# Performance work log

Measured on AMD Instinct MI355X. Metric: run time of the kernel, lower is better.

## Reference

```python
import jax, jax.numpy as jnp
from jax import lax
import numpy as np

B, T, D = 8, 2048, 1024
EPS = 1e-8


def zc_rms(x, g):
    x0 = x - jnp.mean(x, axis=-1, keepdims=True)
    return x0 * jax.lax.rsqrt(jnp.mean(x0 * x0, axis=-1, keepdims=True) + EPS) * g


def l2norm(x):
    return x * jax.lax.rsqrt(jnp.sum(x * x, axis=-1, keepdims=True) + EPS)


def dwconv3(x, w, b):
    # x: [B, T, D]; w: [D, 3] depthwise kernel; b: [D]
    xc = jnp.transpose(x, (0, 2, 1))  # [B, D, T]
    y = lax.conv_general_dilated(xc, w[:, None, :], window_strides=(1,),
                                 padding=[(1, 1)],
                                 dimension_numbers=('NCH', 'OIH', 'NCH'),
                                 feature_group_count=w.shape[0])
    return jnp.transpose(y + b[:, None], (0, 2, 1))  # [B, T, D]


def setup_inputs() -> dict:
    key = jax.random.key(0)
    ks = jax.random.split(key, 16)
    s = 1.0 / np.sqrt(D)
    inp = {
        'x': jax.random.normal(ks[0], (B, T, D), jnp.float32),
        'g1': jnp.ones((D,), jnp.float32),
        'Wq': jax.random.normal(ks[1], (D, D), jnp.float32) * s,
        'bq': jnp.zeros((D,), jnp.float32),
        'Wk': jax.random.normal(ks[2], (D, D), jnp.float32) * s,
        'bk': jnp.zeros((D,), jnp.float32),
        'Wv': jax.random.normal(ks[3], (D, D), jnp.float32) * s,
        'bv': jnp.zeros((D,), jnp.float32),
        'wqc': jax.random.normal(ks[4], (D, 3), jnp.float32) * 0.5,
        'bqc': jnp.zeros((D,), jnp.float32),
        'wkc': jax.random.normal(ks[5], (D, 3), jnp.float32) * 0.5,
        'bkc': jnp.zeros((D,), jnp.float32),
        'wvc': jax.random.normal(ks[6], (D, 3), jnp.float32) * 0.5,
        'bvc': jnp.zeros((D,), jnp.float32),
        'Wa': jax.random.normal(ks[7], (D, D), jnp.float32) * s,
        'ba': jnp.zeros((D,), jnp.float32),
        'Wb': jax.random.normal(ks[8], (D, D), jnp.float32) * s,
        'bb': jnp.zeros((D,), jnp.float32),
        'g2': jnp.ones((D,), jnp.float32),
        'Wp': jax.random.normal(ks[9], (D, D), jnp.float32) * s,
        'bp': jnp.zeros((D,), jnp.float32),
    }
    return inp


def reference(x, g1, Wq, bq, Wk, bk, Wv, bv, wqc, bqc, wkc, bkc, wvc, bvc,
              Wa, ba, Wb, bb, g2, Wp, bp):
    h = zc_rms(x, g1)
    q = jax.nn.sigmoid(dwconv3(h @ Wq + bq, wqc, bqc))
    k = jax.nn.sigmoid(dwconv3(h @ Wk + bk, wkc, bkc))
    v = jax.nn.sigmoid(dwconv3(h @ Wv + bv, wvc, bvc))
    q, k = l2norm(q), l2norm(k)
    delta = q * (k * v)
    delta = jnp.tanh(x @ Wa + ba) * delta + (x @ Wb + bb)
    dhat = zc_rms(delta, g2) @ Wp + bp
    # dropout is identity in eval mode
    return x + jax.nn.sigmoid(jax.nn.silu(dhat)) * dhat
```

## Files before the change

### kernel.cpp

```cpp
#include <hip/hip_runtime.h>
#include <stdint.h>

#define DD 1024
#define TT 2048
#define BBATCH 8
#define MM (BBATCH*TT)

typedef unsigned short u16;
typedef unsigned int   u32;

typedef __attribute__((ext_vector_type(8))) __bf16 bf16x8;
typedef __attribute__((ext_vector_type(4))) float  floatx4;
typedef __attribute__((ext_vector_type(4))) unsigned short u16x4;
typedef __attribute__((ext_vector_type(8))) unsigned short u16x8;
typedef __attribute__((ext_vector_type(4))) unsigned int   u32x4;

__device__ __forceinline__ float b2f(u16 v){
    u32 x = ((u32)v) << 16;
    return __builtin_bit_cast(float, x);
}
__device__ __forceinline__ u16 f2b(float f){
    u32 u = __builtin_bit_cast(u32, f);
    u32 r = (u + 0x7fffu + ((u >> 16) & 1u)) >> 16;
    return (u16)r;
}
__device__ __forceinline__ float sigf(float x){
    return 1.0f / (1.0f + __expf(-x));
}
__device__ __forceinline__ float tanhfast(float x){
    float e = __expf(2.0f * x);
    return 1.0f - 2.0f / (e + 1.0f);
}

__device__ __forceinline__ void g2l16(const u16* g, u16* l){
    __builtin_amdgcn_global_load_lds(
        (const __attribute__((address_space(1))) u32*)g,
        (__attribute__((address_space(3))) u32*)l, 16, 0, 0);
}

__device__ __forceinline__ u32 lds_u32(const u16* p){
    return (u32)(size_t)(const __attribute__((address_space(3))) u16*)p;
}

template<int OFF>
__device__ __forceinline__ bf16x8 dsr(u32 addr){
    u32x4 d;
    asm volatile("ds_read_b128 %0, %1 offset:%2" : "=v"(d) : "v"(addr), "i"(OFF));
    return __builtin_bit_cast(bf16x8, d);
}

template<int BASE>
__device__ __forceinline__ void rd_a8(bf16x8 (&arr)[8], u32 a){
    arr[0]=dsr<BASE+0>(a);    arr[1]=dsr<BASE+64>(a);
    arr[2]=dsr<BASE+2048>(a); arr[3]=dsr<BASE+2112>(a);
    arr[4]=dsr<BASE+4096>(a); arr[5]=dsr<BASE+4160>(a);
    arr[6]=dsr<BASE+6144>(a); arr[7]=dsr<BASE+6208>(a);
}
template<int BASE>
__device__ __forceinline__ void rd_b4(bf16x8 (&arr)[4], u32 a){
    arr[0]=dsr<BASE+0>(a);    arr[1]=dsr<BASE+64>(a);
    arr[2]=dsr<BASE+2048>(a); arr[3]=dsr<BASE+2112>(a);
}

__device__ __forceinline__ void load4bf(const u16* p, float* o){
    u16x4 v = *(const u16x4*)p;
    o[0] = b2f(v.x); o[1] = b2f(v.y); o[2] = b2f(v.z); o[3] = b2f(v.w);
}

__device__ __forceinline__ void wave_reduce2(float& a, float& b){
    #pragma unroll
    for (int m = 32; m; m >>= 1){
        a += __shfl_xor(a, m, 64);
        b += __shfl_xor(b, m, 64);
    }
}

__device__ __forceinline__ void block_reduce2(float& a, float& b, float* red, int tid){
    #pragma unroll
    for (int off = 32; off; off >>= 1){
        a += __shfl_down(a, off, 64);
        b += __shfl_down(b, off, 64);
    }
    __syncthreads();
    if ((tid & 63) == 0){ red[tid >> 6] = a; red[4 + (tid >> 6)] = b; }
    __syncthreads();
    a = red[0] + red[1] + red[2] + red[3];
    b = red[4] + red[5] + red[6] + red[7];
}

__global__ __launch_bounds__(256) void transpose_w(
    const float* __restrict__ s0, const float* __restrict__ s1, const float* __restrict__ s2,
    const float* __restrict__ s3, const float* __restrict__ s4, const float* __restrict__ s5,
    u16* __restrict__ dst_base)
{
    __shared__ u16 tile[32][33];
    const float* srcs[6] = {s0, s1, s2, s3, s4, s5};
    const int z = blockIdx.z;
    const float* src = srcs[z];
    u16* dst = dst_base + (size_t)z * (DD * (size_t)DD);
    const int tx = threadIdx.x, ty = threadIdx.y;
    const int x = blockIdx.x * 32 + tx;
    #pragma unroll
    for (int i = 0; i < 4; i++){
        int y = blockIdx.y * 32 + ty + i * 8;
        tile[ty + i * 8][tx] = f2b(src[(size_t)y * DD + x]);
    }
    __syncthreads();
    const int x2 = blockIdx.y * 32 + tx;
    #pragma unroll
    for (int i = 0; i < 4; i++){
        int y2 = blockIdx.x * 32 + ty + i * 8;
        dst[(size_t)y2 * DD + x2] = tile[tx][ty + i * 8];
    }
}

__global__ __launch_bounds__(256) void prep_wc(
    const float* __restrict__ w0, const float* __restrict__ w1, const float* __restrict__ w2,
    float* __restrict__ wcT)
{
    const float* srcs[3] = {w0, w1, w2};
    const int s = blockIdx.x / 3, tap = blockIdx.x % 3;
    #pragma unroll
    for (int i = 0; i < 4; i++){
        int d = threadIdx.x + i * 256;
        wcT[(s * 3 + tap) * DD + d] = srcs[s][d * 3 + tap];
    }
}

__global__ __launch_bounds__(256) void prep_rows(
    const float* __restrict__ in, const float* __restrict__ g,
    u16* __restrict__ xb, u16* __restrict__ h)
{
    const int tid = threadIdx.x;
    const int w = tid >> 6, lane = tid & 63;
    const int row = blockIdx.x * 4 + w;
    const int d0 = lane * 16;
    const size_t base = (size_t)row * DD + d0;

    float v[16];
    #pragma unroll
    for (int c = 0; c < 4; c++){
        floatx4 t = *(const floatx4*)(in + base + c * 4);
        v[c*4+0] = t.x; v[c*4+1] = t.y; v[c*4+2] = t.z; v[c*4+3] = t.w;
    }
    u16x8 x0, x1;
    #pragma unroll
    for (int j = 0; j < 8; j++){ x0[j] = f2b(v[j]); x1[j] = f2b(v[8+j]); }
    *(u16x8*)(xb + base)     = x0;
    *(u16x8*)(xb + base + 8) = x1;

    float s1 = 0.f, s2 = 0.f;
    #pragma unroll
    for (int j = 0; j < 16; j++){ s1 += v[j]; s2 += v[j]*v[j]; }
    wave_reduce2(s1, s2);
    const float mu = s1 * (1.0f / DD);
    const float ms = fmaxf(s2 * (1.0f / DD) - mu * mu, 0.0f);
    const float sc = rsqrtf(ms + 1e-8f);

    u16x8 o0, o1;
    #pragma unroll
    for (int j = 0; j < 8; j++)  o0[j] = f2b((v[j]     - mu) * sc * g[d0 + j]);
    #pragma unroll
    for (int j = 0; j < 8; j++)  o1[j] = f2b((v[8 + j] - mu) * sc * g[d0 + 8 + j]);
    *(u16x8*)(h + base)     = o0;
    *(u16x8*)(h + base + 8) = o1;
}

struct GemmPtrs {
    const u16*   A[5];
    const u16*   W[5];
    const float* bias[5];
    u16*         out[5];
};

#define BAR()   asm volatile("s_barrier" ::: "memory")
#define LGKM0() asm volatile("s_waitcnt lgkmcnt(0)" ::: "memory")
#define VM8()   asm volatile("s_waitcnt vmcnt(8)" ::: "memory")
#define SB0()   __builtin_amdgcn_sched_barrier(0)
#define PRIO1() __builtin_amdgcn_s_setprio(1)
#define PRIO0() __builtin_amdgcn_s_setprio(0)

template<int IH, int JH>
__device__ __forceinline__ void mm8(floatx4 (&acc)[8][4], const bf16x8 (&af)[8], const bf16x8 (&bf)[4]){
    #pragma unroll
    for (int kk = 0; kk < 2; kk++)
        #pragma unroll
        for (int i = 0; i < 4; i++)
            #pragma unroll
            for (int j = 0; j < 2; j++)
                acc[IH*4+i][JH*2+j] = __builtin_amdgcn_mfma_f32_16x16x32_bf16(
                    af[i*2+kk], bf[j*2+kk], acc[IH*4+i][JH*2+j], 0, 0, 0);
}

template<int MODE>
__global__ __launch_bounds__(512, 2) void gemm_bf16(
    GemmPtrs ptrs, const float* __restrict__ xres, float* __restrict__ dout)
{
    __shared__ alignas(16) u16 lds[65536];

    const int z = blockIdx.z;
    const u16*   __restrict__ A    = ptrs.A[z];
    const u16*   __restrict__ W    = ptrs.W[z];
    const float* __restrict__ bias = ptrs.bias[z];
    u16* __restrict__ Cout = ptrs.out[z];

    const int tid  = threadIdx.x;
    const int wave = tid >> 6, lane = tid & 63;
    const int quad = lane >> 4, l16 = lane & 15;
    const int wrow = wave >> 2, wcol = wave & 3;
    const int bm = blockIdx.x * 256;
    const int bn = blockIdx.y * 256;

    const int coloff = ((tid & 7) * 8) ^ (((tid >> 5) & 1) << 4);
    const u16* srcA = A + (size_t)(bm + (tid >> 3)) * DD + coloff;
    const u16* srcB = W + (size_t)(bn + (tid >> 3)) * DD + coloff;

    #define STAGE_A(T,H) do{ \
        u16* _d = &lds[(((T)&1)*2 + (H))*8192 + tid*8]; \
        const u16* _g = srcA + (size_t)(H)*128*DD + (size_t)(((T)&15)*64); \
        g2l16(_g, _d); g2l16(_g + (size_t)64*DD, _d + 4096); }while(0)
    #define STAGE_B(T,H) do{ \
        u16* _d = &lds[32768 + (((T)&1)*2 + (H))*8192 + tid*8]; \
        const u16* _g = srcB + (size_t)(H)*128*DD + (size_t)(((T)&15)*64); \
        g2l16(_g, _d); g2l16(_g + (size_t)64*DD, _d + 4096); }while(0)

    const u32 swz = (u32)((quad * 16) ^ (((l16 >> 2) & 1) << 5));
    const u32 lbase = lds_u32(&lds[0]);
    u32 addr_a = lbase + (u32)(wrow * 8192 + l16 * 128) + swz;
    u32 addr_b = lbase + 65536u + (u32)(wcol * 4096 + l16 * 128) + swz;

    floatx4 acc[8][4];
    #pragma unroll
    for (int i = 0; i < 8; i++)
        #pragma unroll
        for (int j = 0; j < 4; j++)
            acc[i][j] = (floatx4){0.f, 0.f, 0.f, 0.f};

    STAGE_A(0,0); STAGE_B(0,0); STAGE_B(0,1); STAGE_A(0,1); STAGE_A(1,0); STAGE_B(1,0);
    VM8(); BAR();

    bf16x8 af0[8], af1[8], bf0[4], bf1[4];

    for (int t = 0; t < 16; ++t){
        rd_a8<0>(af0, addr_a);
        rd_b4<0>(bf0, addr_b);
        STAGE_B(t+1, 1);
        BAR(); LGKM0(); SB0();
        PRIO1(); mm8<0,0>(acc, af0, bf0); PRIO0(); SB0();
        VM8(); BAR();
        rd_b4<16384>(bf1, addr_b);
        STAGE_A(t+1, 1);
        BAR(); LGKM0(); SB0();
        PRIO1(); mm8<0,1>(acc, af0, bf1); PRIO0(); SB0();
        VM8(); BAR();
        rd_a8<16384>(af1, addr_a);
        STAGE_A(t+2, 0);
        BAR(); LGKM0(); SB0();
        PRIO1(); mm8<1,0>(acc, af1, bf0); PRIO0(); SB0();
        STAGE_B(t+2, 0);
        PRIO1(); mm8<1,1>(acc, af1, bf1); PRIO0(); SB0();
        VM8(); BAR();
        addr_a ^= 32768u; addr_b ^= 32768u;
    }

    #undef STAGE_A
    #undef STAGE_B

    float bj[4];
    #pragma unroll
    for (int j = 0; j < 4; j++)
        bj[j] = bias[bn + (j >= 2 ? 128 : 0) + wcol * 32 + (j & 1) * 16 + l16];

    #pragma unroll
    for (int i = 0; i < 8; i++){
        const int row0 = bm + (i >= 4 ? 128 : 0) + wrow * 64 + (i & 3) * 16 + quad * 4;
        #pragma unroll
        for (int j = 0; j < 4; j++){
            const int col = bn + (j >= 2 ? 128 : 0) + wcol * 32 + (j & 1) * 16 + l16;
            #pragma unroll
            for (int r = 0; r < 4; r++){
                size_t idx = (size_t)(row0 + r) * DD + col;
                float zv = acc[i][j][r] + bj[j];
                if (MODE == 0){
                    Cout[idx] = f2b(zv);
                } else {
                    float sl = zv * sigf(zv);
                    dout[idx] = xres[idx] + sigf(sl) * zv;
                }
            }
        }
    }
}

__global__ __launch_bounds__(256) void mid_fuse(
    const u16* __restrict__ q0, const u16* __restrict__ k0, const u16* __restrict__ v0,
    const u16* __restrict__ a0, const u16* __restrict__ b0,
    const float* __restrict__ wcT,
    const float* __restrict__ bqc, const float* __restrict__ bkc, const float* __restrict__ bvc,
    const float* __restrict__ g2, u16* __restrict__ uout)
{
    __shared__ float red[8];
    const int row = blockIdx.x;
    const int t   = row & (TT - 1);
    const int tid = threadIdx.x;
    const int d0  = tid * 4;
    const size_t base = (size_t)row * DD + d0;
    const bool hm = (t > 0), hp = (t < TT - 1);

    float q[4], k[4], v[4];
    {
        const u16*   srcs[3] = {q0, k0, v0};
        const float* bs[3]   = {bqc, bkc, bvc};
        float* outs[3]       = {q, k, v};
        #pragma unroll
        for (int s = 0; s < 3; s++){
            float cm[4], cc[4], cp[4];
            load4bf(srcs[s] + base, cc);
            if (hm) load4bf(srcs[s] + base - DD, cm);
            else { cm[0]=0.f; cm[1]=0.f; cm[2]=0.f; cm[3]=0.f; }
            if (hp) load4bf(srcs[s] + base + DD, cp);
            else { cp[0]=0.f; cp[1]=0.f; cp[2]=0.f; cp[3]=0.f; }
            const float* wt = wcT + s * 3 * DD + d0;
            const float* bb = bs[s] + d0;
            #pragma unroll
            for (int j = 0; j < 4; j++){
                float y = cm[j] * wt[j] + cc[j] * wt[DD + j] + cp[j] * wt[2 * DD + j] + bb[j];
                outs[s][j] = sigf(y);
            }
        }
    }

    float sq = 0.f, sk = 0.f;
    #pragma unroll
    for (int j = 0; j < 4; j++){ sq += q[j] * q[j]; sk += k[j] * k[j]; }
    block_reduce2(sq, sk, red, tid);
    const float rq = rsqrtf(sq + 1e-8f), rk = rsqrtf(sk + 1e-8f);

    float av[4], bv[4];
    load4bf(a0 + base, av);
    load4bf(b0 + base, bv);

    float dl[4], s1 = 0.f, s2 = 0.f;
    #pragma unroll
    for (int j = 0; j < 4; j++){
        float d = (q[j] * rq) * (k[j] * rk) * v[j];
        d = tanhfast(av[j]) * d + bv[j];
        dl[j] = d; s1 += d; s2 += d * d;
    }
    block_reduce2(s1, s2, red, tid);
    const float mu = s1 * (1.0f / DD);
    const float ms = fmaxf(s2 * (1.0f / DD) - mu * mu, 0.0f);
    const float sc = rsqrtf(ms + 1e-8f);

    u16x4 ov;
    ov.x = f2b((dl[0] - mu) * sc * g2[d0 + 0]);
    ov.y = f2b((dl[1] - mu) * sc * g2[d0 + 1]);
    ov.z = f2b((dl[2] - mu) * sc * g2[d0 + 2]);
    ov.w = f2b((dl[3] - mu) * sc * g2[d0 + 3]);
    *(u16x4*)(uout + base) = ov;
}

extern "C" void kernel_launch(void* const* d_in, const int* in_sizes, int n_in,
                              void* d_out, int out_size, void* d_ws, size_t ws_size,
                              hipStream_t stream)
{
    const float* x   = (const float*)d_in[0];
    const float* g1  = (const float*)d_in[1];
    const float* Wq  = (const float*)d_in[2];
    const float* bq  = (const float*)d_in[3];
    const float* Wk  = (const float*)d_in[4];
    const float* bk  = (const float*)d_in[5];
    const float* Wv  = (const float*)d_in[6];
    const float* bv  = (const float*)d_in[7];
    const float* wqc = (const float*)d_in[8];
    const float* bqc = (const float*)d_in[9];
    const float* wkc = (const float*)d_in[10];
    const float* bkc = (const float*)d_in[11];
    const float* wvc = (const float*)d_in[12];
    const float* bvc = (const float*)d_in[13];
    const float* Wa  = (const float*)d_in[14];
    const float* ba  = (const float*)d_in[15];
    const float* Wb  = (const float*)d_in[16];
    const float* bb  = (const float*)d_in[17];
    const float* g2  = (const float*)d_in[18];
    const float* Wp  = (const float*)d_in[19];
    const float* bp  = (const float*)d_in[20];

    u16* ws = (u16*)d_ws;
    const size_t WSZ = (size_t)DD * DD;
    const size_t TSZ = (size_t)MM * DD;
    u16* WT = ws;
    float* wcT = (float*)(ws + 6 * WSZ);
    u16* xb = ws + 6 * WSZ + 32768;
    u16* h  = xb + TSZ;
    u16* q0 = h  + TSZ;
    u16* k0 = q0 + TSZ;
    u16* v0 = k0 + TSZ;
    u16* a0 = v0 + TSZ;
    u16* b0 = a0 + TSZ;
    u16* u  = h;

    transpose_w<<<dim3(32, 32, 6), dim3(32, 8, 1), 0, stream>>>(Wq, Wk, Wv, Wa, Wb, Wp, WT);
    prep_wc<<<dim3(9), dim3(256), 0, stream>>>(wqc, wkc, wvc, wcT);
    prep_rows<<<dim3(MM / 4), dim3(256), 0, stream>>>(x, g1, xb, h);

    GemmPtrs p0;
    p0.A[0] = h;  p0.W[0] = WT + 0 * WSZ; p0.bias[0] = bq; p0.out[0] = q0;
    p0.A[1] = h;  p0.W[1] = WT + 1 * WSZ; p0.bias[1] = bk; p0.out[1] = k0;
    p0.A[2] = h;  p0.W[2] = WT + 2 * WSZ; p0.bias[2] = bv; p0.out[2] = v0;
    p0.A[3] = xb; p0.W[3] = WT + 3 * WSZ; p0.bias[3] = ba; p0.out[3] = a0;
    p0.A[4] = xb; p0.W[4] = WT + 4 * WSZ; p0.bias[4] = bb; p0.out[4] = b0;
    gemm_bf16<0><<<dim3(64, 4, 5), dim3(512), 0, stream>>>(p0, nullptr, nullptr);

    mid_fuse<<<dim3(MM), dim3(256), 0, stream>>>(q0, k0, v0, a0, b0,
                                                 wcT, bqc, bkc, bvc, g2, u);

    GemmPtrs p1;
    for (int i = 0; i < 5; i++){ p1.A[i] = u; p1.W[i] = WT + 5 * WSZ; p1.bias[i] = bp; p1.out[i] = nullptr; }
    gemm_bf16<1><<<dim3(64, 4, 1), dim3(512), 0, stream>>>(p1, x, (float*)d_out);
}
```

Measured before the change: 470.3 us.

## Use full XOR LDS swizzle, prefetch next fragments, and trim GEMM barriers

The GEMM's LDS layout changes to a full 8-way XOR swizzle on 16-byte chunks, with two base addresses per wave, to reduce bank conflicts on ds_read_b128. Fragment reads for the next k-step are issued during the current MFMA phases, so LDS latency overlaps compute. Several barriers are removed and the global-load wait tightens from vmcnt(8) to vmcnt(4). This risks race conditions on the double-buffered LDS if the barrier removal breaks ordering, and adds register pressure from the live prefetched fragments.

```diff
diff --git a/kernel.cpp b/kernel.cpp
--- a/kernel.cpp
+++ b/kernel.cpp
@@ -50,16 +50,16 @@
 }
 
 template<int BASE>
-__device__ __forceinline__ void rd_a8(bf16x8 (&arr)[8], u32 a){
-    arr[0]=dsr<BASE+0>(a);    arr[1]=dsr<BASE+64>(a);
-    arr[2]=dsr<BASE+2048>(a); arr[3]=dsr<BASE+2112>(a);
-    arr[4]=dsr<BASE+4096>(a); arr[5]=dsr<BASE+4160>(a);
-    arr[6]=dsr<BASE+6144>(a); arr[7]=dsr<BASE+6208>(a);
+__device__ __forceinline__ void rd_a8(bf16x8 (&arr)[8], u32 a0, u32 a1){
+    arr[0]=dsr<BASE+0>(a0);    arr[1]=dsr<BASE+0>(a1);
+    arr[2]=dsr<BASE+2048>(a0); arr[3]=dsr<BASE+2048>(a1);
+    arr[4]=dsr<BASE+4096>(a0); arr[5]=dsr<BASE+4096>(a1);
+    arr[6]=dsr<BASE+6144>(a0); arr[7]=dsr<BASE+6144>(a1);
 }
 template<int BASE>
-__device__ __forceinline__ void rd_b4(bf16x8 (&arr)[4], u32 a){
-    arr[0]=dsr<BASE+0>(a);    arr[1]=dsr<BASE+64>(a);
-    arr[2]=dsr<BASE+2048>(a); arr[3]=dsr<BASE+2112>(a);
+__device__ __forceinline__ void rd_b4(bf16x8 (&arr)[4], u32 a0, u32 a1){
+    arr[0]=dsr<BASE+0>(a0);    arr[1]=dsr<BASE+0>(a1);
+    arr[2]=dsr<BASE+2048>(a0); arr[3]=dsr<BASE+2048>(a1);
 }
 
 __device__ __forceinline__ void load4bf(const u16* p, float* o){
@@ -175,7 +175,7 @@
 
 #define BAR()   asm volatile("s_barrier" ::: "memory")
 #define LGKM0() asm volatile("s_waitcnt lgkmcnt(0)" ::: "memory")
-#define VM8()   asm volatile("s_waitcnt vmcnt(8)" ::: "memory")
+#define VM4()   asm volatile("s_waitcnt vmcnt(4)" ::: "memory")
 #define SB0()   __builtin_amdgcn_sched_barrier(0)
 #define PRIO1() __builtin_amdgcn_s_setprio(1)
 #define PRIO0() __builtin_amdgcn_s_setprio(0)
@@ -211,7 +211,7 @@
     const int bm = blockIdx.x * 256;
     const int bn = blockIdx.y * 256;
 
-    const int coloff = ((tid & 7) * 8) ^ (((tid >> 5) & 1) << 4);
+    const int coloff = (((tid & 7) ^ ((tid >> 3) & 7)) * 8);
     const u16* srcA = A + (size_t)(bm + (tid >> 3)) * DD + coloff;
     const u16* srcB = W + (size_t)(bn + (tid >> 3)) * DD + coloff;
 
@@ -224,10 +224,14 @@
         const u16* _g = srcB + (size_t)(H)*128*DD + (size_t)(((T)&15)*64); \
         g2l16(_g, _d); g2l16(_g + (size_t)64*DD, _d + 4096); }while(0)
 
-    const u32 swz = (u32)((quad * 16) ^ (((l16 >> 2) & 1) << 5));
     const u32 lbase = lds_u32(&lds[0]);
-    u32 addr_a = lbase + (u32)(wrow * 8192 + l16 * 128) + swz;
-    u32 addr_b = lbase + 65536u + (u32)(wcol * 4096 + l16 * 128) + swz;
+    const u32 rowb  = (u32)(l16 * 128);
+    const u32 sw0   = (u32)(((quad    ) ^ (l16 & 7)) << 4);
+    const u32 sw1   = (u32)(((quad + 4) ^ (l16 & 7)) << 4);
+    u32 addr_a0 = lbase + (u32)(wrow * 8192) + rowb + sw0;
+    u32 addr_a1 = lbase + (u32)(wrow * 8192) + rowb + sw1;
+    u32 addr_b0 = lbase + 65536u + (u32)(wcol * 4096) + rowb + sw0;
+    u32 addr_b1 = lbase + 65536u + (u32)(wcol * 4096) + rowb + sw1;
 
     floatx4 acc[8][4];
     #pragma unroll
@@ -237,31 +241,35 @@
             acc[i][j] = (floatx4){0.f, 0.f, 0.f, 0.f};
 
     STAGE_A(0,0); STAGE_B(0,0); STAGE_B(0,1); STAGE_A(0,1); STAGE_A(1,0); STAGE_B(1,0);
-    VM8(); BAR();
-
+    VM4(); BAR();
     bf16x8 af0[8], af1[8], bf0[4], bf1[4];
+    rd_a8<0>(af0, addr_a0, addr_a1);
+    rd_b4<0>(bf0, addr_b0, addr_b1);
 
     for (int t = 0; t < 16; ++t){
-        rd_a8<0>(af0, addr_a);
-        rd_b4<0>(bf0, addr_b);
         STAGE_B(t+1, 1);
-        BAR(); LGKM0(); SB0();
+        BAR();
+        LGKM0(); SB0();
         PRIO1(); mm8<0,0>(acc, af0, bf0); PRIO0(); SB0();
-        VM8(); BAR();
-        rd_b4<16384>(bf1, addr_b);
+        rd_b4<16384>(bf1, addr_b0, addr_b1);
         STAGE_A(t+1, 1);
-        BAR(); LGKM0(); SB0();
+        LGKM0(); SB0();
         PRIO1(); mm8<0,1>(acc, af0, bf1); PRIO0(); SB0();
-        VM8(); BAR();
-        rd_a8<16384>(af1, addr_a);
+        rd_a8<16384>(af1, addr_a0, addr_a1);
+        VM4(); BAR();
         STAGE_A(t+2, 0);
-        BAR(); LGKM0(); SB0();
+        BAR();
+        LGKM0(); SB0();
         PRIO1(); mm8<1,0>(acc, af1, bf0); PRIO0(); SB0();
+        rd_a8<0>(af0, addr_a0 ^ 32768u, addr_a1 ^ 32768u);
+        rd_b4<0>(bf0, addr_b0 ^ 32768u, addr_b1 ^ 32768u);
         STAGE_B(t+2, 0);
         PRIO1(); mm8<1,1>(acc, af1, bf1); PRIO0(); SB0();
-        VM8(); BAR();
-        addr_a ^= 32768u; addr_b ^= 32768u;
-    }
+        VM4(); BAR();
+        addr_a0 ^= 32768u; addr_a1 ^= 32768u;
+        addr_b0 ^= 32768u; addr_b1 ^= 32768u;
+    }
+    asm volatile("s_waitcnt vmcnt(0) lgkmcnt(0)" ::: "memory");
 
     #undef STAGE_A
     #undef STAGE_B
```

After: 453.9 us. 1.04x faster.
